# Kernel tuning notes

Measured on AMD Instinct MI355X. Metric: run time of the kernel, lower is better.

Reference implementation:

```python
import jax, jax.numpy as jnp
import numpy as np

DG = 8   # deformable groups
KK = 9   # 3x3 kernel positions


def conv3x3(x, w, b):
    # x: [B,C,H,W], w: [O,I,3,3] -> SAME conv, stride 1
    y = jax.lax.conv_general_dilated(x, w, (1, 1), 'SAME',
                                     dimension_numbers=('NCHW', 'OIHW', 'NCHW'))
    return y + b[None, :, None, None]


def modulated_deform_conv(x, offset, mask, w, b):
    # x: [B,C,H,W]; offset: [B,DG,KK,2,H,W] (dy,dx per group/kernel-pos);
    # mask: [B,DG,KK,H,W]; w: [O,C,3,3]; groups=1, stride=1, pad=1, dil=1.
    B, C, H, W = x.shape
    cg = C // DG  # channels per deformable group
    dy = offset[:, :, :, 0]  # [B,DG,KK,H,W]
    dx = offset[:, :, :, 1]
    ky, kx = jnp.meshgrid(jnp.arange(3), jnp.arange(3), indexing='ij')
    ky = (ky.reshape(KK) - 1).astype(x.dtype)  # kernel y offsets (pad=1)
    kx = (kx.reshape(KK) - 1).astype(x.dtype)
    py = dy + jnp.arange(H, dtype=x.dtype).reshape(1, 1, 1, H, 1) + ky.reshape(1, 1, KK, 1, 1)
    px = dx + jnp.arange(W, dtype=x.dtype).reshape(1, 1, 1, 1, W) + kx.reshape(1, 1, KK, 1, 1)
    y0 = jnp.floor(py)
    x0 = jnp.floor(px)
    ly = py - y0  # bilinear fractions
    lx = px - x0
    y0i = y0.astype(jnp.int32)
    x0i = x0.astype(jnp.int32)
    xf = x.reshape(B, DG, cg, H * W)

    def gather(yi, xi):
        # zero padding outside the image (per-corner validity)
        valid = ((yi >= 0) & (yi < H) & (xi >= 0) & (xi < W)).astype(x.dtype)
        idx = jnp.clip(yi, 0, H - 1) * W + jnp.clip(xi, 0, W - 1)  # [B,DG,KK,H,W]
        g = jnp.take_along_axis(xf, idx.reshape(B, DG, 1, KK * H * W), axis=-1)
        return g.reshape(B, DG, cg, KK, H, W) * valid[:, :, None]

    v = (((1 - ly) * (1 - lx))[:, :, None] * gather(y0i, x0i)
         + ((1 - ly) * lx)[:, :, None] * gather(y0i, x0i + 1)
         + (ly * (1 - lx))[:, :, None] * gather(y0i + 1, x0i)
         + (ly * lx)[:, :, None] * gather(y0i + 1, x0i + 1))
    v = (v * mask[:, :, None]).reshape(B, C, KK, H, W)  # modulated im2col
    out = jnp.einsum('bckhw,ock->bohw', v, w.reshape(w.shape[0], C, KK))
    return out + b[None, :, None, None]


def setup_inputs() -> dict:
    key = jax.random.key(0)
    ks = jax.random.split(key, 6)
    B, C, H, W = 8, 64, 128, 128
    f = lambda k, s: jax.random.normal(k, s, dtype=jnp.float32)
    return {
        'cat_fea': f(ks[0], (B, C, H, W)),
        'f_fea': f(ks[1], (B, C, H, W)),
        'w_off2d': f(ks[2], (C, C, 3, 3)) * 0.05,
        'b_off2d': jnp.zeros((C,), jnp.float32),
        'w_coff': f(ks[3], (3 * DG * KK, C, 3, 3)) * 0.01,  # small => near-zero offsets, as in DCNv2Pack init
        'b_coff': jnp.zeros((3 * DG * KK,), jnp.float32),
        'w_dconv': f(ks[4], (C, C, 3, 3)) * 0.05,
        'b_dconv': jnp.zeros((C,), jnp.float32),
    }


def reference(cat_fea, f_fea, w_off2d, b_off2d, w_coff, b_coff, w_dconv, b_dconv):
    # offset1 = self.off2d_1(cat_fea)
    offset_feat = conv3x3(cat_fea, w_off2d, b_off2d)
    # DCNv2Pack: conv_offset on the extra feature, chunk into o1,o2,mask
    off = conv3x3(offset_feat, w_coff, b_coff)  # [B, 3*DG*KK, H, W]
    o1, o2, m = jnp.split(off, 3, axis=1)
    B, _, H, W = off.shape
    # offset = cat(o1,o2); CUDA kernel reads channel ((g*KK+i)*2 + {0:y,1:x})
    offset = jnp.concatenate([o1, o2], axis=1).reshape(B, DG, KK, 2, H, W)
    mask = jax.nn.sigmoid(m).reshape(B, DG, KK, H, W)
    return modulated_deform_conv(f_fea, offset, mask, w_dconv, b_dconv)
```

## Files before the change

### kernel.cpp

```cpp
#include <hip/hip_runtime.h>
#include <math.h>

typedef __attribute__((ext_vector_type(4))) float f32x4;
typedef __attribute__((ext_vector_type(8))) short bf16x8;

#define HH 128
#define WW 128
#define HWSZ 16384
#define BHW 131072
#define BB 8

__device__ __forceinline__ float bf2f(ushort u) {
    union { uint i; float f; } x; x.i = ((uint)u) << 16; return x.f;
}
__device__ __forceinline__ ushort f2bf(float f) {
    union { float f; uint i; } x; x.f = f;
    uint r = (x.i + 0x7fffu + ((x.i >> 16) & 1u)) >> 16;
    return (ushort)r;
}

__global__ __launch_bounds__(256) void to_gp_bf16(const float* __restrict__ x,
                                                  ushort* __restrict__ y) {
    __shared__ ushort lds[64][66];
    int blk = blockIdx.x;
    int b = blk >> 8;
    int hw0 = (blk & 255) << 6;
    int t = threadIdx.x;
    int lane = t & 63;
    int q = t >> 6;
#pragma unroll
    for (int i = 0; i < 16; i++) {
        int c = i * 4 + q;
        lds[c][lane] = f2bf(x[((size_t)(b * 64 + c) << 14) + hw0 + lane]);
    }
    __syncthreads();
#pragma unroll
    for (int it = 0; it < 2; it++) {
        int id = it * 256 + t;
        int cg = id >> 6;
        int px = id & 63;
        uint pk[4];
#pragma unroll
        for (int j = 0; j < 4; j++)
            pk[j] = (uint)lds[cg * 8 + 2 * j][px] | ((uint)lds[cg * 8 + 2 * j + 1][px] << 16);
        *(uint4*)(y + ((((size_t)b * 8 + cg) << 14) + hw0 + px) * 8) = *(uint4*)pk;
    }
}

__global__ __launch_bounds__(256) void prep_wa(const float* __restrict__ w,
                                               ushort* __restrict__ wa, int Co, int Co_pad) {
    int idx = blockIdx.x * 256 + threadIdx.x;
    if (idx >= Co_pad * 576) return;
    int co = idx / 576, r = idx % 576;
    int kk = r >> 6, ci = r & 63;
    ushort v = 0;
    if (co < Co) v = f2bf(w[(co * 64 + ci) * 9 + kk]);
    wa[idx] = v;
}

template<int NCO, int MODE>
__global__ __launch_bounds__(256, 3) void conv_gemm2_k(
    const ushort* __restrict__ xt, const ushort* __restrict__ wa,
    const float* __restrict__ bias, ushort* __restrict__ y,
    uint* __restrict__ dyxp, ushort* __restrict__ mpl, int Cout) {
    __shared__ ushort Al[NCO * 64 * 64];
    __shared__ ushort Bt[64 * 64];
    int t = threadIdx.x;
    int orig = blockIdx.x;
    int blk = (orig & 7) * 256 + (orig >> 3);
    int b = blk >> 8;
    int h = (blk >> 1) & 127;
    int w0 = (blk & 1) << 6;
    int lane = t & 63;
    int wv = t >> 6;
    int lg = lane >> 4;
    int lr = lane & 15;
    int rs = (lr & 7) << 4;
    int asw = ((lane & 7) ^ (lane >> 3)) << 4;
    const char* wab = (const char*)wa;

    f32x4 acc[NCO][4];
#pragma unroll
    for (int n = 0; n < NCO; n++)
#pragma unroll
        for (int j = 0; j < 4; j++) acc[n][j] = f32x4{0, 0, 0, 0};

#pragma unroll 1
    for (int kk = 0; kk < 9; kk++) {
        int ky = kk / 3;
        int kx = kk - ky * 3;
        __syncthreads();
#pragma unroll
        for (int a = 0; a < 2 * NCO; a++) {
            int rb = wv * (NCO * 16) + a * 8;
            const char* g = wab + (size_t)(rb + (lane >> 3)) * 1152 + kk * 128 + asw;
            __builtin_amdgcn_global_load_lds(
                (const __attribute__((address_space(1))) void*)g,
                (__attribute__((address_space(3))) void*)((char*)Al + rb * 128),
                16, 0, 0);
        }
        int hy = h + ky - 1;
        int wx = w0 + lane + kx - 1;
        bool val = ((unsigned)hy < 128u) && ((unsigned)wx < 128u);
        uint4 v0 = {0u, 0u, 0u, 0u}, v1 = {0u, 0u, 0u, 0u};
        if (val) {
            const ushort* gb = xt + ((((size_t)b * 8 + wv) << 14) + (hy << 7) + wx) * 8;
            v0 = *(const uint4*)gb;
            v1 = *(const uint4*)(gb + (4ull << 17));
        }
        int swl = (lane & 7) << 4;
        *(uint4*)((char*)Bt + lane * 128 + ((wv * 16) ^ swl)) = v0;
        *(uint4*)((char*)Bt + lane * 128 + (((wv + 4) * 16) ^ swl)) = v1;
        __syncthreads();
#pragma unroll
        for (int n = 0; n < NCO; n++) {
            int ar = n * 64 + wv * 16 + lr;
            bf16x8 a0 = *(const bf16x8*)((char*)Al + ar * 128 + ((lg * 16) ^ rs));
            bf16x8 a1 = *(const bf16x8*)((char*)Al + ar * 128 + ((lg * 16 + 64) ^ rs));
#pragma unroll
            for (int j = 0; j < 4; j++) {
                int pr = j * 16 + lr;
                bf16x8 b0 = *(const bf16x8*)((char*)Bt + pr * 128 + ((lg * 16) ^ rs));
                bf16x8 b1 = *(const bf16x8*)((char*)Bt + pr * 128 + ((lg * 16 + 64) ^ rs));
                acc[n][j] = __builtin_amdgcn_mfma_f32_16x16x32_bf16(a0, b0, acc[n][j], 0, 0, 0);
                acc[n][j] = __builtin_amdgcn_mfma_f32_16x16x32_bf16(a1, b1, acc[n][j], 0, 0, 0);
            }
        }
    }

#pragma unroll
    for (int n = 0; n < NCO; n++) {
        int co_g = n * 64 + wv * 16 + lg * 4;
        if (co_g < Cout) {
            float bs[4];
#pragma unroll
            for (int r = 0; r < 4; r++) bs[r] = bias[co_g + r];
#pragma unroll
            for (int j = 0; j < 4; j++) {
                int pxl = j * 16 + lr;
                int hw = (h << 7) + w0 + pxl;
                int bhw = (b << 14) + hw;
                if (MODE == 0) {
                    int cg = co_g >> 3, cs = co_g & 7;
                    uint2 s2;
                    s2.x = (uint)f2bf(acc[n][j][0] + bs[0]) | ((uint)f2bf(acc[n][j][1] + bs[1]) << 16);
                    s2.y = (uint)f2bf(acc[n][j][2] + bs[2]) | ((uint)f2bf(acc[n][j][3] + bs[3]) << 16);
                    *(uint2*)(y + ((((size_t)b * 8 + cg) << 14) + hw) * 8 + cs) = s2;
                } else if (co_g < 144) {
                    int p0 = co_g >> 1;
                    uint u0 = (uint)f2bf(acc[n][j][0] + bs[0]) | ((uint)f2bf(acc[n][j][1] + bs[1]) << 16);
                    uint u1 = (uint)f2bf(acc[n][j][2] + bs[2]) | ((uint)f2bf(acc[n][j][3] + bs[3]) << 16);
                    dyxp[(size_t)p0 * BHW + bhw] = u0;
                    dyxp[(size_t)(p0 + 1) * BHW + bhw] = u1;
                } else {
#pragma unroll
                    for (int r = 0; r < 4; r++) {
                        float f = 1.f / (1.f + __expf(-(acc[n][j][r] + bs[r])));
                        mpl[(size_t)(co_g - 144 + r) * BHW + bhw] = f2bf(f);
                    }
                }
            }
        }
    }
}

__global__ __launch_bounds__(256, 3) void deform_pipe_k(
    const ushort* __restrict__ xg, const uint* __restrict__ dyxp,
    const ushort* __restrict__ mpl, const ushort* __restrict__ wa,
    const float* __restrict__ bias, float* __restrict__ out) {
    __shared__ ushort Bl[2 * 64 * 192];
    int t = threadIdx.x;
    int orig = blockIdx.x;
    int blk = (orig & 7) * 256 + (orig >> 3);
    int b = blk >> 8;
    int h = (blk >> 1) & 127;
    int w0 = (blk & 1) << 6;
    int lane = t & 63;
    int wv = t >> 6;
    int lg = lane >> 4;
    int lr = lane & 15;
    int wgl = w0 + lane;
    int bhw = (b << 14) + (h << 7) + wgl;

    uint4 st[6];

#define SAMPLE(KR) do {                                                         \
    _Pragma("unroll")                                                           \
    for (int i = 0; i < 6; i++) {                                               \
        int u = i * 4 + wv;                                                     \
        int dg = u / 3;                                                         \
        int q = u - dg * 3;                                                     \
        int p = dg * 9 + (KR) * 3 + q;                                          \
        uint dyx = dyxp[(size_t)p * BHW + bhw];                                 \
        float m = bf2f(mpl[(size_t)p * BHW + bhw]);                             \
        float dy = bf2f((ushort)(dyx & 0xffff));                                \
        float dx = bf2f((ushort)(dyx >> 16));                                   \
        float py = dy + (float)(h + (KR) - 1);                                  \
        float px_ = dx + (float)(wgl + q - 1);                                  \
        float fy = floorf(py), fx = floorf(px_);                                \
        int y0 = (int)fy, x0 = (int)fx;                                         \
        int y1 = y0 + 1, x1 = x0 + 1;                                           \
        float ly = py - fy, lx = px_ - fx;                                      \
        bool vy0 = (unsigned)y0 < (unsigned)HH, vy1 = (unsigned)y1 < (unsigned)HH; \
        bool vx0 = (unsigned)x0 < (unsigned)WW, vx1 = (unsigned)x1 < (unsigned)WW; \
        float w00 = (vy0 && vx0) ? (1.f - ly) * (1.f - lx) * m : 0.f;           \
        float w01 = (vy0 && vx1) ? (1.f - ly) * lx * m : 0.f;                   \
        float w10 = (vy1 && vx0) ? ly * (1.f - lx) * m : 0.f;                   \
        float w11 = (vy1 && vx1) ? ly * lx * m : 0.f;                           \
        int y0c = min(max(y0, 0), HH - 1), y1c = min(max(y1, 0), HH - 1);       \
        int x0c = min(max(x0, 0), WW - 1), x1c = min(max(x1, 0), WW - 1);       \
        const ushort* gb = xg + (((size_t)b * 8 + dg) << 17);                   \
        uint4 q00 = *(const uint4*)(gb + ((y0c << 7) + x0c) * 8);               \
        uint4 q01 = *(const uint4*)(gb + ((y0c << 7) + x1c) * 8);               \
        uint4 q10 = *(const uint4*)(gb + ((y1c << 7) + x0c) * 8);               \
        uint4 q11 = *(const uint4*)(gb + ((y1c << 7) + x1c) * 8);               \
        const ushort* u00 = (const ushort*)&q00;                                \
        const ushort* u01 = (const ushort*)&q01;                                \
        const ushort* u10 = (const ushort*)&q10;                                \
        const ushort* u11 = (const ushort*)&q11;                                \
        uint pk[4];                                                             \
        _Pragma("unroll")                                                       \
        for (int c2 = 0; c2 < 4; c2++) {                                        \
            float v0 = w00 * bf2f(u00[2*c2])   + w01 * bf2f(u01[2*c2])          \
                     + w10 * bf2f(u10[2*c2])   + w11 * bf2f(u11[2*c2]);         \
            float v1 = w00 * bf2f(u00[2*c2+1]) + w01 * bf2f(u01[2*c2+1])        \
                     + w10 * bf2f(u10[2*c2+1]) + w11 * bf2f(u11[2*c2+1]);       \
            pk[c2] = (uint)f2bf(v0) | ((uint)f2bf(v1) << 16);                   \
        }                                                                       \
        st[i] = *(uint4*)pk;                                                    \
    } } while (0)

#define STAGE_WRITE(BI) do {                                                    \
    _Pragma("unroll")                                                           \
    for (int i = 0; i < 6; i++) {                                               \
        int u = i * 4 + wv;                                                     \
        int dg = u / 3;                                                         \
        int q = u - dg * 3;                                                     \
        int kb = (q * 128 + dg * 16) ^ ((lane & 7) << 4);                       \
        *(uint4*)((char*)Bl + (BI) * 24576 + lane * 384 + kb) = st[i];          \
    } } while (0)

    f32x4 acc[4] = {f32x4{0,0,0,0}, f32x4{0,0,0,0}, f32x4{0,0,0,0}, f32x4{0,0,0,0}};

#define MFMA_CHUNK(CH, BI) do {                                                 \
    _Pragma("unroll")                                                           \
    for (int c = 0; c < 6; c++) {                                               \
        bf16x8 a = *(const bf16x8*)(wa +                                        \
            (size_t)(wv * 16 + lr) * 576 + (CH) * 192 + c * 32 + lg * 8);       \
        _Pragma("unroll")                                                       \
        for (int j = 0; j < 4; j++) {                                           \
            int px = j * 16 + lr;                                               \
            int kb = (c * 64 + lg * 16) ^ ((px & 7) << 4);                      \
            bf16x8 bv = *(const bf16x8*)((char*)Bl + (BI) * 24576 + px * 384 + kb); \
            acc[j] = __builtin_amdgcn_mfma_f32_16x16x32_bf16(a, bv, acc[j], 0, 0, 0); \
        }                                                                       \
    } } while (0)

    SAMPLE(0);
    STAGE_WRITE(0);
    __syncthreads();

    SAMPLE(1);
    MFMA_CHUNK(0, 0);
    __syncthreads();
    STAGE_WRITE(1);
    __syncthreads();

    SAMPLE(2);
    MFMA_CHUNK(1, 1);
    __syncthreads();
    STAGE_WRITE(0);
    __syncthreads();

    MFMA_CHUNK(2, 0);

    int co_g = wv * 16 + lg * 4;
    float bs[4];
#pragma unroll
    for (int r = 0; r < 4; r++) bs[r] = bias[co_g + r];
#pragma unroll
    for (int j = 0; j < 4; j++) {
        int pxl = j * 16 + lr;
        int hw = (h << 7) + w0 + pxl;
#pragma unroll
        for (int r = 0; r < 4; r++) {
            out[((size_t)(b * 64 + co_g + r) << 14) + hw] = acc[j][r] + bs[r];
        }
    }
#undef SAMPLE
#undef STAGE_WRITE
#undef MFMA_CHUNK
}

extern "C" void kernel_launch(void* const* d_in, const int* in_sizes, int n_in,
                              void* d_out, int out_size, void* d_ws, size_t ws_size,
                              hipStream_t stream) {
    const float* cat_fea = (const float*)d_in[0];
    const float* f_fea   = (const float*)d_in[1];
    const float* w_off2d = (const float*)d_in[2];
    const float* b_off2d = (const float*)d_in[3];
    const float* w_coff  = (const float*)d_in[4];
    const float* b_coff  = (const float*)d_in[5];
    const float* w_dconv = (const float*)d_in[6];
    const float* b_dconv = (const float*)d_in[7];
    float* out = (float*)d_out;

    ushort* x1t      = (ushort*)d_ws;
    ushort* xft      = x1t + 8388608;
    ushort* off_feat = xft + 8388608;
    uint*   dyxp     = (uint*)(off_feat + 8388608);
    ushort* mpl      = (ushort*)(dyxp + 9437184);
    ushort* wa1      = mpl + 9437184;
    ushort* wa2      = wa1 + 36864;
    ushort* wad      = wa2 + 147456;

    to_gp_bf16<<<2048, 256, 0, stream>>>(cat_fea, x1t);
    to_gp_bf16<<<2048, 256, 0, stream>>>(f_fea, xft);
    prep_wa<<<(64 * 576 + 255) / 256, 256, 0, stream>>>(w_off2d, wa1, 64, 64);
    prep_wa<<<(256 * 576 + 255) / 256, 256, 0, stream>>>(w_coff, wa2, 216, 256);
    prep_wa<<<(64 * 576 + 255) / 256, 256, 0, stream>>>(w_dconv, wad, 64, 64);

    conv_gemm2_k<1, 0><<<2048, 256, 0, stream>>>(x1t, wa1, b_off2d, off_feat,
                                                 nullptr, nullptr, 64);
    conv_gemm2_k<4, 1><<<2048, 256, 0, stream>>>(off_feat, wa2, b_coff, nullptr,
                                                 dyxp, mpl, 216);
    deform_pipe_k<<<2048, 256, 0, stream>>>(xft, dyxp, mpl, wad, b_dconv, out);
}
```

Baseline: 151.8 us.

## Feed bilinear samples directly into MFMA B-fragments, dropping LDS staging

The deformable conv kernel now has each lane sample exactly the 8 channels its MFMA B operand needs, so the im2col tile stays in registers. This removes the LDS double buffer and all block barriers, and raises the launch-bounds occupancy target from 3 to 4. In exchange, each wave now covers all 64 output channels for 16 pixels, so weight A-fragments are reloaded from global memory four times per k-chunk. Sampling latency is also no longer overlapped with MFMA through the staged pipeline.

```diff
diff --git a/kernel.cpp b/kernel.cpp
--- a/kernel.cpp
+++ b/kernel.cpp
@@ -164,11 +164,10 @@
     }
 }
 
-__global__ __launch_bounds__(256, 3) void deform_pipe_k(
+__global__ __launch_bounds__(256, 4) void deform_reg_k(
     const ushort* __restrict__ xg, const uint* __restrict__ dyxp,
     const ushort* __restrict__ mpl, const ushort* __restrict__ wa,
     const float* __restrict__ bias, float* __restrict__ out) {
-    __shared__ ushort Bl[2 * 64 * 192];
     int t = threadIdx.x;
     int orig = blockIdx.x;
     int blk = (orig & 7) * 256 + (orig >> 3);
@@ -179,117 +178,73 @@
     int wv = t >> 6;
     int lg = lane >> 4;
     int lr = lane & 15;
-    int wgl = w0 + lane;
-    int bhw = (b << 14) + (h << 7) + wgl;
-
-    uint4 st[6];
-
-#define SAMPLE(KR) do {                                                         \
-    _Pragma("unroll")                                                           \
-    for (int i = 0; i < 6; i++) {                                               \
-        int u = i * 4 + wv;                                                     \
-        int dg = u / 3;                                                         \
-        int q = u - dg * 3;                                                     \
-        int p = dg * 9 + (KR) * 3 + q;                                          \
-        uint dyx = dyxp[(size_t)p * BHW + bhw];                                 \
-        float m = bf2f(mpl[(size_t)p * BHW + bhw]);                             \
-        float dy = bf2f((ushort)(dyx & 0xffff));                                \
-        float dx = bf2f((ushort)(dyx >> 16));                                   \
-        float py = dy + (float)(h + (KR) - 1);                                  \
-        float px_ = dx + (float)(wgl + q - 1);                                  \
-        float fy = floorf(py), fx = floorf(px_);                                \
-        int y0 = (int)fy, x0 = (int)fx;                                         \
-        int y1 = y0 + 1, x1 = x0 + 1;                                           \
-        float ly = py - fy, lx = px_ - fx;                                      \
-        bool vy0 = (unsigned)y0 < (unsigned)HH, vy1 = (unsigned)y1 < (unsigned)HH; \
-        bool vx0 = (unsigned)x0 < (unsigned)WW, vx1 = (unsigned)x1 < (unsigned)WW; \
-        float w00 = (vy0 && vx0) ? (1.f - ly) * (1.f - lx) * m : 0.f;           \
-        float w01 = (vy0 && vx1) ? (1.f - ly) * lx * m : 0.f;                   \
-        float w10 = (vy1 && vx0) ? ly * (1.f - lx) * m : 0.f;                   \
-        float w11 = (vy1 && vx1) ? ly * lx * m : 0.f;                           \
-        int y0c = min(max(y0, 0), HH - 1), y1c = min(max(y1, 0), HH - 1);       \
-        int x0c = min(max(x0, 0), WW - 1), x1c = min(max(x1, 0), WW - 1);       \
-        const ushort* gb = xg + (((size_t)b * 8 + dg) << 17);                   \
-        uint4 q00 = *(const uint4*)(gb + ((y0c << 7) + x0c) * 8);               \
-        uint4 q01 = *(const uint4*)(gb + ((y0c << 7) + x1c) * 8);               \
-        uint4 q10 = *(const uint4*)(gb + ((y1c << 7) + x0c) * 8);               \
-        uint4 q11 = *(const uint4*)(gb + ((y1c << 7) + x1c) * 8);               \
-        const ushort* u00 = (const ushort*)&q00;                                \
-        const ushort* u01 = (const ushort*)&q01;                                \
-        const ushort* u10 = (const ushort*)&q10;                                \
-        const ushort* u11 = (const ushort*)&q11;                                \
-        uint pk[4];                                                             \
-        _Pragma("unroll")                                                       \
-        for (int c2 = 0; c2 < 4; c2++) {                                        \
-            float v0 = w00 * bf2f(u00[2*c2])   + w01 * bf2f(u01[2*c2])          \
-                     + w10 * bf2f(u10[2*c2])   + w11 * bf2f(u11[2*c2]);         \
-            float v1 = w00 * bf2f(u00[2*c2+1]) + w01 * bf2f(u01[2*c2+1])        \
-                     + w10 * bf2f(u10[2*c2+1]) + w11 * bf2f(u11[2*c2+1]);       \
-            pk[c2] = (uint)f2bf(v0) | ((uint)f2bf(v1) << 16);                   \
-        }                                                                       \
-        st[i] = *(uint4*)pk;                                                    \
-    } } while (0)
-
-#define STAGE_WRITE(BI) do {                                                    \
-    _Pragma("unroll")                                                           \
-    for (int i = 0; i < 6; i++) {                                               \
-        int u = i * 4 + wv;                                                     \
-        int dg = u / 3;                                                         \
-        int q = u - dg * 3;                                                     \
-        int kb = (q * 128 + dg * 16) ^ ((lane & 7) << 4);                       \
-        *(uint4*)((char*)Bl + (BI) * 24576 + lane * 384 + kb) = st[i];          \
-    } } while (0)
+    int wabs = w0 + wv * 16 + lr;
+    int bhw = (b << 14) + (h << 7) + wabs;
 
     f32x4 acc[4] = {f32x4{0,0,0,0}, f32x4{0,0,0,0}, f32x4{0,0,0,0}, f32x4{0,0,0,0}};
 
-#define MFMA_CHUNK(CH, BI) do {                                                 \
-    _Pragma("unroll")                                                           \
-    for (int c = 0; c < 6; c++) {                                               \
-        bf16x8 a = *(const bf16x8*)(wa +                                        \
-            (size_t)(wv * 16 + lr) * 576 + (CH) * 192 + c * 32 + lg * 8);       \
-        _Pragma("unroll")                                                       \
-        for (int j = 0; j < 4; j++) {                                           \
-            int px = j * 16 + lr;                                               \
-            int kb = (c * 64 + lg * 16) ^ ((px & 7) << 4);                      \
-            bf16x8 bv = *(const bf16x8*)((char*)Bl + (BI) * 24576 + px * 384 + kb); \
-            acc[j] = __builtin_amdgcn_mfma_f32_16x16x32_bf16(a, bv, acc[j], 0, 0, 0); \
-        }                                                                       \
-    } } while (0)
-
-    SAMPLE(0);
-    STAGE_WRITE(0);
-    __syncthreads();
-
-    SAMPLE(1);
-    MFMA_CHUNK(0, 0);
-    __syncthreads();
-    STAGE_WRITE(1);
-    __syncthreads();
-
-    SAMPLE(2);
-    MFMA_CHUNK(1, 1);
-    __syncthreads();
-    STAGE_WRITE(0);
-    __syncthreads();
-
-    MFMA_CHUNK(2, 0);
-
-    int co_g = wv * 16 + lg * 4;
-    float bs[4];
-#pragma unroll
-    for (int r = 0; r < 4; r++) bs[r] = bias[co_g + r];
-#pragma unroll
-    for (int j = 0; j < 4; j++) {
-        int pxl = j * 16 + lr;
-        int hw = (h << 7) + w0 + pxl;
+#pragma unroll
+    for (int c = 0; c < 18; c++) {
+        const int dg_l = ((c & 1) << 2);
+        const int tap = c >> 1;
+        const int ky = tap / 3;
+        const int kx = tap - ky * 3;
+        int dg = dg_l + lg;
+        int p = dg * 9 + tap;
+        uint dyx = dyxp[(size_t)p * BHW + bhw];
+        float m = bf2f(mpl[(size_t)p * BHW + bhw]);
+        float dy = bf2f((ushort)(dyx & 0xffff));
+        float dx = bf2f((ushort)(dyx >> 16));
+        float py = dy + (float)(h + ky - 1);
+        float px_ = dx + (float)(wabs + kx - 1);
+        float fy = floorf(py), fx = floorf(px_);
+        int y0 = (int)fy, x0 = (int)fx;
+        int y1 = y0 + 1, x1 = x0 + 1;
+        float ly = py - fy, lx = px_ - fx;
+        bool vy0 = (unsigned)y0 < (unsigned)HH, vy1 = (unsigned)y1 < (unsigned)HH;
+        bool vx0 = (unsigned)x0 < (unsigned)WW, vx1 = (unsigned)x1 < (unsigned)WW;
+        float w00 = (vy0 && vx0) ? (1.f - ly) * (1.f - lx) * m : 0.f;
+        float w01 = (vy0 && vx1) ? (1.f - ly) * lx * m : 0.f;
+        float w10 = (vy1 && vx0) ? ly * (1.f - lx) * m : 0.f;
+        float w11 = (vy1 && vx1) ? ly * lx * m : 0.f;
+        int y0c = min(max(y0, 0), HH - 1), y1c = min(max(y1, 0), HH - 1);
+        int x0c = min(max(x0, 0), WW - 1), x1c = min(max(x1, 0), WW - 1);
+        const ushort* gb = xg + (((size_t)b * 8 + dg) << 17);
+        uint4 q00 = *(const uint4*)(gb + ((y0c << 7) + x0c) * 8);
+        uint4 q01 = *(const uint4*)(gb + ((y0c << 7) + x1c) * 8);
+        uint4 q10 = *(const uint4*)(gb + ((y1c << 7) + x0c) * 8);
+        uint4 q11 = *(const uint4*)(gb + ((y1c << 7) + x1c) * 8);
+        const ushort* u00 = (const ushort*)&q00;
+        const ushort* u01 = (const ushort*)&q01;
+        const ushort* u10 = (const ushort*)&q10;
+        const ushort* u11 = (const ushort*)&q11;
+        uint pk[4];
+#pragma unroll
+        for (int c2 = 0; c2 < 4; c2++) {
+            float v0 = w00 * bf2f(u00[2*c2])   + w01 * bf2f(u01[2*c2])
+                     + w10 * bf2f(u10[2*c2])   + w11 * bf2f(u11[2*c2]);
+            float v1 = w00 * bf2f(u00[2*c2+1]) + w01 * bf2f(u01[2*c2+1])
+                     + w10 * bf2f(u10[2*c2+1]) + w11 * bf2f(u11[2*c2+1]);
+            pk[c2] = (uint)f2bf(v0) | ((uint)f2bf(v1) << 16);
+        }
+        bf16x8 bfrag = *(bf16x8*)pk;
+        const ushort* wac = wa + c * 32 + lg * 8;
+#pragma unroll
+        for (int n = 0; n < 4; n++) {
+            bf16x8 a = *(const bf16x8*)(wac + (size_t)(n * 16 + lr) * 576);
+            acc[n] = __builtin_amdgcn_mfma_f32_16x16x32_bf16(a, bfrag, acc[n], 0, 0, 0);
+        }
+    }
+
+    int hw = (h << 7) + wabs;
+#pragma unroll
+    for (int n = 0; n < 4; n++) {
+        int co_g = n * 16 + lg * 4;
 #pragma unroll
         for (int r = 0; r < 4; r++) {
-            out[((size_t)(b * 64 + co_g + r) << 14) + hw] = acc[j][r] + bs[r];
-        }
-    }
-#undef SAMPLE
-#undef STAGE_WRITE
-#undef MFMA_CHUNK
+            out[((size_t)(b * 64 + co_g + r) << 14) + hw] = acc[n][r] + bias[co_g + r];
+        }
+    }
 }
 
 extern "C" void kernel_launch(void* const* d_in, const int* in_sizes, int n_in,
@@ -324,5 +279,5 @@
                                                  nullptr, nullptr, 64);
     conv_gemm2_k<4, 1><<<2048, 256, 0, stream>>>(off_feat, wa2, b_coff, nullptr,
                                                  dyxp, mpl, 216);
-    deform_pipe_k<<<2048, 256, 0, stream>>>(xft, dyxp, mpl, wad, b_dconv, out);
-}
+    deform_reg_k<<<2048, 256, 0, stream>>>(xft, dyxp, mpl, wad, b_dconv, out);
+}
```

Measured after the change: 188.4 us. 24.1% more time.
